# Kernel tuning notes

Hardware: AMD Instinct MI355X
Metric: run time of the kernel (lower is better)

Reference implementation:

```python
import jax, jax.numpy as jnp
import numpy as np


def setup_inputs() -> dict:
    key = jax.random.key(0)
    k1, k2 = jax.random.split(key)
    B, Te, Td, D = 8, 2048, 2048, 256
    encoder_outputs = jax.random.normal(k1, (B, Te, D), dtype=jnp.float32)
    decoder_outputs = jax.random.normal(k2, (B, Td, D), dtype=jnp.float32)
    return {"encoder_outputs": encoder_outputs, "decoder_outputs": decoder_outputs}


def reference(encoder_outputs, decoder_outputs):
    # score[b, e, t] = enc[b, e, :] . dec[b, t, :]   -> [B, Te, Td]
    score = jnp.einsum('bed,btd->bet', encoder_outputs, decoder_outputs)
    # softmax over the encoder-time axis (axis=1), matching K.softmax(..., axis=1)
    attn = jax.nn.softmax(score, axis=1)
    # context[b, t, d] = sum_e attn[b, e, t] * enc[b, e, d]
    # (original does expand_dims + broadcast-mul + sum; einsum is the same math)
    context = jnp.einsum('bet,bed->btd', attn, encoder_outputs)
    return jnp.concatenate([decoder_outputs, context], axis=-1)  # [B, Td, 2D]
```

## Files before the change

kernel.cpp:

```cpp
#include <hip/hip_runtime.h>


#define B_   8
#define TE   2048
#define TD   2048
#define D_   256
#define NIT  32

typedef _Float16 f16x8 __attribute__((ext_vector_type(8)));
typedef float f32x4 __attribute__((ext_vector_type(4)));

__device__ __forceinline__ unsigned pk2(float a, float b) {
  unsigned short ua = __builtin_bit_cast(unsigned short, (_Float16)a);
  unsigned short ub = __builtin_bit_cast(unsigned short, (_Float16)b);
  return (unsigned)ua | ((unsigned)ub << 16);
}

#define GLOAD16(gsrc, ldst)                                                  \
  __builtin_amdgcn_global_load_lds(                                          \
      (const __attribute__((address_space(1))) unsigned int*)(const void*)(gsrc), \
      (__attribute__((address_space(3))) unsigned int*)(void*)(ldst), 16, 0, 0)

__global__ __launch_bounds__(256) void prep_fused(const float* __restrict__ enc,
                                                  _Float16* __restrict__ encK,
                                                  _Float16* __restrict__ encVt) {
  __shared__ float tile[64][65];
  int bid = blockIdx.x;
  int b = bid >> 7, r = bid & 127;
  int et = r >> 2, dt = r & 3;
  int e0 = et * 64, d0 = dt * 64;
  int tx = threadIdx.x & 63, ty = threadIdx.x >> 6;
  const float* src = enc + ((size_t)b * TE + e0) * D_ + d0;
#pragma unroll
  for (int i = 0; i < 16; ++i)
    tile[i * 4 + ty][tx] = src[(size_t)(i * 4 + ty) * D_ + tx];
  __syncthreads();

  _Float16* kout = encK + ((size_t)b * TE + e0) * D_ + d0;
#pragma unroll
  for (int i = 0; i < 2; ++i) {
    int ci = i * 256 + threadIdx.x;
    int e = ci >> 3, xl = ci & 7;
    int xs = xl ^ (e & 7);
    const float* s8 = &tile[e][xs * 8];
    f16x8 h;
#pragma unroll
    for (int j = 0; j < 8; ++j) h[j] = (_Float16)s8[j];
    *(f16x8*)(kout + (size_t)e * D_ + xl * 8) = h;
  }
#pragma unroll
  for (int i = 0; i < 2; ++i) {
    int u = i * 256 + threadIdx.x;
    int y = u & 3, d_loc = (u >> 2) & 63, ctl = u >> 8;
    int s = (d_loc >> 1) & 3;
    int ebase = ctl * 32 + ((y ^ s) << 3);
    f16x8 h;
#pragma unroll
    for (int j = 0; j < 8; ++j) h[j] = (_Float16)tile[ebase + j][d_loc];
    size_t o = (((size_t)b * 64 + et * 2 + ctl) * 256 + d0 + d_loc) * 32 + y * 8;
    *(f16x8*)(encVt + o) = h;
  }
}

__global__ __launch_bounds__(512, 2) void luong_main(
    const _Float16* __restrict__ encK,
    const _Float16* __restrict__ encVt,
    const float* __restrict__ dec,
    float* __restrict__ out) {
  extern __shared__ char lds[];
  const int tid = threadIdx.x;
  const int lane = tid & 63, wave = tid >> 6;
  const int wr = wave >> 2, wc = wave & 3;
  const int g = lane >> 4, c = lane & 15;

  int bidl = (blockIdx.x & 7) * 32 + (blockIdx.x >> 3);
  const int b = bidl >> 5;
  const int q0 = (bidl & 31) * 64;
  const int t = q0 + wc * 16 + c;

  const float* decB = dec + (size_t)b * TD * D_;
  float* outB = out + (size_t)b * TD * (2 * D_);

  const _Float16* kbase = encK + ((size_t)b * TE + wr * 1024) * D_;
  const _Float16* vbase = encVt + ((size_t)b * 64 + wr * 32) * 8192;

  auto STAGE = [&](int buf, int it) {
    char* Kd = lds + (size_t)(buf * 2 + wr) * 32768;
    char* Vd = Kd + 16384;
    const _Float16* ks = kbase + (size_t)it * 8192;
    const _Float16* vs = vbase + (size_t)it * 8192;
#pragma unroll
    for (int q = 0; q < 4; ++q) {
      int chunk = wc * 256 + q * 64 + lane;
      GLOAD16(ks + (size_t)chunk * 8, Kd + wc * 4096 + q * 1024);
      GLOAD16(vs + (size_t)chunk * 8, Vd + wc * 4096 + q * 1024);
    }
  };

  STAGE(0, 0);
  STAGE(1, 1);

#pragma unroll
  for (int i = 0; i < 8; ++i) {
    int ci = tid + 512 * i;
    int rr = ci >> 6, d4 = (ci & 63) << 2;
    *(float4*)(outB + (size_t)(q0 + rr) * 512 + d4) =
        *(const float4*)(decB + (size_t)(q0 + rr) * 256 + d4);
  }

  f16x8 qh[8], ql[8];
  {
    const float* qrow = decB + (size_t)t * D_;
#pragma unroll
    for (int dc = 0; dc < 8; ++dc) {
      float4 v0 = *(const float4*)(qrow + dc * 32 + 8 * g);
      float4 v1 = *(const float4*)(qrow + dc * 32 + 8 * g + 4);
      float f[8] = {v0.x, v0.y, v0.z, v0.w, v1.x, v1.y, v1.z, v1.w};
      f16x8 H, L;
#pragma unroll
      for (int j = 0; j < 8; ++j) {
        _Float16 h = (_Float16)f[j];
        H[j] = h;
        L[j] = (_Float16)(f[j] - (float)h);
      }
      qh[dc] = H; ql[dc] = L;
    }
  }

  float m_run = -INFINITY, l_run = 0.f;
  f32x4 ctx[16];
#pragma unroll
  for (int i = 0; i < 16; ++i) ctx[i] = (f32x4){0.f, 0.f, 0.f, 0.f};

  f32x4 sA, sB;
  f16x8 bfrag;

  auto QK = [&](const char* Kb) {
    sA = (f32x4){0.f, 0.f, 0.f, 0.f};
    sB = (f32x4){0.f, 0.f, 0.f, 0.f};
    const int el0 = c, el1 = 16 + c;
#pragma unroll
    for (int dc = 0; dc < 8; ++dc) {
      int x = dc * 4 + g;
      int xsw = (x & 24) | ((x ^ el0) & 7);
      f16x8 k0 = *(const f16x8*)(Kb + el0 * 512 + (xsw << 4));
      f16x8 k1 = *(const f16x8*)(Kb + el1 * 512 + (xsw << 4));
      sA = __builtin_amdgcn_mfma_f32_16x16x32_f16(k0, qh[dc], sA, 0, 0, 0);
      sA = __builtin_amdgcn_mfma_f32_16x16x32_f16(k0, ql[dc], sA, 0, 0, 0);
      sB = __builtin_amdgcn_mfma_f32_16x16x32_f16(k1, qh[dc], sB, 0, 0, 0);
      sB = __builtin_amdgcn_mfma_f32_16x16x32_f16(k1, ql[dc], sB, 0, 0, 0);
    }
  };

  auto PV = [&](const char* Vb) {
#pragma unroll
    for (int dt = 0; dt < 16; ++dt) {
      int row = dt * 16 + c;
      f16x8 af = *(const f16x8*)(Vb + row * 64 + ((g ^ ((row >> 1) & 3)) << 4));
      ctx[dt] = __builtin_amdgcn_mfma_f32_16x16x32_f16(af, bfrag, ctx[dt], 0, 0, 0);
    }
  };

  auto SOFTMAX = [&]() {
    float vmax = fmaxf(fmaxf(fmaxf(sA[0], sA[1]), fmaxf(sA[2], sA[3])),
                       fmaxf(fmaxf(sB[0], sB[1]), fmaxf(sB[2], sB[3])));
    vmax = fmaxf(vmax, __shfl_xor(vmax, 16, 64));
    vmax = fmaxf(vmax, __shfl_xor(vmax, 32, 64));
    if (!__all(vmax <= m_run + 8.0f)) {
      float m_new = fmaxf(m_run, vmax);
      float alpha = __expf(m_run - m_new);
      l_run *= alpha;
#pragma unroll
      for (int i = 0; i < 16; ++i) ctx[i] *= alpha;
      m_run = m_new;
    }
    float p0 = __expf(sA[0] - m_run), p1 = __expf(sA[1] - m_run);
    float p2 = __expf(sA[2] - m_run), p3 = __expf(sA[3] - m_run);
    float p4 = __expf(sB[0] - m_run), p5 = __expf(sB[1] - m_run);
    float p6 = __expf(sB[2] - m_run), p7 = __expf(sB[3] - m_run);
    float ps = ((p0 + p1) + (p2 + p3)) + ((p4 + p5) + (p6 + p7));
    ps += __shfl_xor(ps, 16, 64);
    ps += __shfl_xor(ps, 32, 64);
    l_run += ps;
    unsigned w00 = pk2(p0, p1), w10 = pk2(p2, p3);
    unsigned w01 = pk2(p4, p5), w11 = pk2(p6, p7);
    int srcA = (2 * (g & 1)) * 16 + c, srcB = srcA + 16;
    int y0 = __shfl((int)w00, srcA, 64), y1 = __shfl((int)w10, srcA, 64);
    int y2 = __shfl((int)w00, srcB, 64), y3 = __shfl((int)w10, srcB, 64);
    int z0 = __shfl((int)w01, srcA, 64), z1 = __shfl((int)w11, srcA, 64);
    int z2 = __shfl((int)w01, srcB, 64), z3 = __shfl((int)w11, srcB, 64);
    int4 bi = (g >> 1) ? make_int4(z0, z1, z2, z3) : make_int4(y0, y1, y2, y3);
    bfrag = __builtin_bit_cast(f16x8, bi);
  };

  asm volatile("s_waitcnt vmcnt(8)" ::: "memory");
  __builtin_amdgcn_sched_barrier(0);
  __builtin_amdgcn_s_barrier();
  __builtin_amdgcn_sched_barrier(0);

#pragma unroll 2
  for (int it = 0; it < NIT; ++it) {
    const int cur = it & 1;
    const char* bufC = lds + (size_t)(cur * 2 + wr) * 32768;

    __builtin_amdgcn_s_setprio(1);
    QK(bufC);
    __builtin_amdgcn_s_setprio(0);
    SOFTMAX();
    __builtin_amdgcn_s_setprio(1);
    PV(bufC + 16384);
    __builtin_amdgcn_s_setprio(0);

    asm volatile("s_waitcnt lgkmcnt(0)" ::: "memory");
    __builtin_amdgcn_sched_barrier(0);
    __builtin_amdgcn_s_barrier();
    __builtin_amdgcn_sched_barrier(0);

    if (it + 2 < NIT) {
      STAGE(cur, it + 2);
      asm volatile("s_waitcnt vmcnt(8)" ::: "memory");
    } else {
      asm volatile("s_waitcnt vmcnt(0)" ::: "memory");
    }
    __builtin_amdgcn_sched_barrier(0);
    __builtin_amdgcn_s_barrier();
    __builtin_amdgcn_sched_barrier(0);
  }

  float* mlb = (float*)(lds + 130048);
  if (lane < 16) {
    mlb[((wr * 4 + wc) * 16 + c) * 2 + 0] = m_run;
    mlb[((wr * 4 + wc) * 16 + c) * 2 + 1] = l_run;
  }
  __syncthreads();
  float m_o = mlb[(((1 - wr) * 4 + wc) * 16 + c) * 2 + 0];
  float l_o = mlb[(((1 - wr) * 4 + wc) * 16 + c) * 2 + 1];
  float M = fmaxf(m_run, m_o);
  float fme = __expf(m_run - M);
  float L = l_run * fme + l_o * __expf(m_o - M);
  float invL = 1.0f / L;

  float* Xb = (float*)lds + wc * 4352;
  if (wr == 1) {
#pragma unroll
    for (int dt = 0; dt < 16; ++dt)
#pragma unroll
      for (int r = 0; r < 4; ++r) {
        int d = dt * 16 + 4 * g + r;
        Xb[d * 17 + c] = ctx[dt][r] * fme;
      }
  }
  __syncthreads();
  if (wr == 0) {
    float* orow = outB + (size_t)t * 512 + 256;
#pragma unroll
    for (int dt = 0; dt < 16; ++dt) {
      float4 v;
      float vv[4];
#pragma unroll
      for (int r = 0; r < 4; ++r) {
        int d = dt * 16 + 4 * g + r;
        vv[r] = (ctx[dt][r] * fme + Xb[d * 17 + c]) * invL;
      }
      v.x = vv[0]; v.y = vv[1]; v.z = vv[2]; v.w = vv[3];
      *(float4*)(orow + dt * 16 + 4 * g) = v;
    }
  }
}

extern "C" void kernel_launch(void* const* d_in, const int* in_sizes, int n_in,
                              void* d_out, int out_size, void* d_ws, size_t ws_size,
                              hipStream_t stream) {
  const float* enc = (const float*)d_in[0];
  const float* dec = (const float*)d_in[1];
  float* out = (float*)d_out;
  (void)in_sizes; (void)n_in; (void)out_size; (void)ws_size;

  _Float16* encK  = (_Float16*)d_ws;
  _Float16* encVt = (_Float16*)((char*)d_ws + 8388608);

  prep_fused<<<1024, 256, 0, stream>>>(enc, encK, encVt);
  luong_main<<<256, 512, 131072, stream>>>(encK, encVt, dec, out);
}
```

Measured before the change: 157.3 us.

## Restructure attention main loop: 2 query tiles per wave, K prefetch, 16x16x16 PV

Halves the block to 4 waves, each handling two 16-row query tiles so every K/V fragment read from LDS feeds twice as many MFMAs. The QK product for the next iteration is issued before the softmax and PV of the current one, with a triple-buffered K ring and a double-buffered V ring. This software-pipelines the loop and removes the shuffle-based P transpose by using 16x16x16 MFMAs with a re-laid-out V tile. Register pressure rises sharply (two ctx accumulators per wave) and LDS per block grows to 160KB, which lowers occupancy to one block per CU.

```diff
diff --git a/kernel.cpp b/kernel.cpp
--- a/kernel.cpp
+++ b/kernel.cpp
@@ -8,6 +8,7 @@
 #define NIT  32
 
 typedef _Float16 f16x8 __attribute__((ext_vector_type(8)));
+typedef _Float16 f16x4 __attribute__((ext_vector_type(4)));
 typedef float f32x4 __attribute__((ext_vector_type(4)));
 
 __device__ __forceinline__ unsigned pk2(float a, float b) {
@@ -51,18 +52,20 @@
 #pragma unroll
   for (int i = 0; i < 2; ++i) {
     int u = i * 256 + threadIdx.x;
-    int y = u & 3, d_loc = (u >> 2) & 63, ctl = u >> 8;
-    int s = (d_loc >> 1) & 3;
-    int ebase = ctl * 32 + ((y ^ s) << 3);
+    int gpos = u & 3, d_loc = (u >> 2) & 63, ctl = u >> 8;
+    int gs = gpos ^ ((d_loc >> 1) & 3);
+    int eb = ctl * 32 + 4 * gs;
     f16x8 h;
 #pragma unroll
-    for (int j = 0; j < 8; ++j) h[j] = (_Float16)tile[ebase + j][d_loc];
-    size_t o = (((size_t)b * 64 + et * 2 + ctl) * 256 + d0 + d_loc) * 32 + y * 8;
+    for (int j = 0; j < 4; ++j) h[j] = (_Float16)tile[eb + j][d_loc];
+#pragma unroll
+    for (int j = 0; j < 4; ++j) h[4 + j] = (_Float16)tile[eb + 16 + j][d_loc];
+    size_t o = (((size_t)b * 64 + et * 2 + ctl) * 256 + d0 + d_loc) * 32 + gpos * 8;
     *(f16x8*)(encVt + o) = h;
   }
 }
 
-__global__ __launch_bounds__(512, 2) void luong_main(
+__global__ __launch_bounds__(256, 1) void luong_main(
     const _Float16* __restrict__ encK,
     const _Float16* __restrict__ encVt,
     const float* __restrict__ dec,
@@ -70,13 +73,13 @@
   extern __shared__ char lds[];
   const int tid = threadIdx.x;
   const int lane = tid & 63, wave = tid >> 6;
-  const int wr = wave >> 2, wc = wave & 3;
+  const int wr = wave >> 1, tw = wave & 1;
   const int g = lane >> 4, c = lane & 15;
 
   int bidl = (blockIdx.x & 7) * 32 + (blockIdx.x >> 3);
   const int b = bidl >> 5;
   const int q0 = (bidl & 31) * 64;
-  const int t = q0 + wc * 16 + c;
+  const int tbase = q0 + tw * 32;
 
   const float* decB = dec + (size_t)b * TD * D_;
   float* outB = out + (size_t)b * TD * (2 * D_);
@@ -84,33 +87,38 @@
   const _Float16* kbase = encK + ((size_t)b * TE + wr * 1024) * D_;
   const _Float16* vbase = encVt + ((size_t)b * 64 + wr * 32) * 8192;
 
-  auto STAGE = [&](int buf, int it) {
-    char* Kd = lds + (size_t)(buf * 2 + wr) * 32768;
-    char* Vd = Kd + 16384;
-    const _Float16* ks = kbase + (size_t)it * 8192;
-    const _Float16* vs = vbase + (size_t)it * 8192;
-#pragma unroll
-    for (int q = 0; q < 4; ++q) {
-      int chunk = wc * 256 + q * 64 + lane;
-      GLOAD16(ks + (size_t)chunk * 8, Kd + wc * 4096 + q * 1024);
-      GLOAD16(vs + (size_t)chunk * 8, Vd + wc * 4096 + q * 1024);
-    }
+  char* grpK = lds + (size_t)wr * 81920;
+  char* grpV = grpK + 49152;
+
+  auto KSTAGE = [&](int slot, int it) {
+    char* Kd = grpK + slot * 16384 + tw * 8192;
+    const _Float16* ks = kbase + (size_t)it * 8192 + tw * 4096;
+#pragma unroll
+    for (int q = 0; q < 8; ++q)
+      GLOAD16(ks + q * 512 + lane * 8, Kd + q * 1024);
   };
-
-  STAGE(0, 0);
-  STAGE(1, 1);
-
-#pragma unroll
-  for (int i = 0; i < 8; ++i) {
-    int ci = tid + 512 * i;
+  auto VSTAGE = [&](int slot, int it) {
+    char* Vd = grpV + slot * 16384 + tw * 8192;
+    const _Float16* vs = vbase + (size_t)it * 8192 + tw * 4096;
+#pragma unroll
+    for (int q = 0; q < 8; ++q)
+      GLOAD16(vs + q * 512 + lane * 8, Vd + q * 1024);
+  };
+
+  KSTAGE(0, 0); VSTAGE(0, 0); KSTAGE(1, 1); VSTAGE(1, 1); KSTAGE(2, 2);
+
+#pragma unroll
+  for (int i = 0; i < 16; ++i) {
+    int ci = tid + 256 * i;
     int rr = ci >> 6, d4 = (ci & 63) << 2;
     *(float4*)(outB + (size_t)(q0 + rr) * 512 + d4) =
         *(const float4*)(decB + (size_t)(q0 + rr) * 256 + d4);
   }
 
-  f16x8 qh[8], ql[8];
-  {
-    const float* qrow = decB + (size_t)t * D_;
+  f16x8 qh[2][8], ql[2][8];
+#pragma unroll
+  for (int tt = 0; tt < 2; ++tt) {
+    const float* qrow = decB + (size_t)(tbase + tt * 16 + c) * D_;
 #pragma unroll
     for (int dc = 0; dc < 8; ++dc) {
       float4 v0 = *(const float4*)(qrow + dc * 32 + 8 * g);
@@ -123,147 +131,178 @@
         H[j] = h;
         L[j] = (_Float16)(f[j] - (float)h);
       }
-      qh[dc] = H; ql[dc] = L;
-    }
-  }
-
-  float m_run = -INFINITY, l_run = 0.f;
-  f32x4 ctx[16];
-#pragma unroll
-  for (int i = 0; i < 16; ++i) ctx[i] = (f32x4){0.f, 0.f, 0.f, 0.f};
-
-  f32x4 sA, sB;
-  f16x8 bfrag;
-
-  auto QK = [&](const char* Kb) {
-    sA = (f32x4){0.f, 0.f, 0.f, 0.f};
-    sB = (f32x4){0.f, 0.f, 0.f, 0.f};
-    const int el0 = c, el1 = 16 + c;
-#pragma unroll
-    for (int dc = 0; dc < 8; ++dc) {
-      int x = dc * 4 + g;
-      int xsw = (x & 24) | ((x ^ el0) & 7);
-      f16x8 k0 = *(const f16x8*)(Kb + el0 * 512 + (xsw << 4));
-      f16x8 k1 = *(const f16x8*)(Kb + el1 * 512 + (xsw << 4));
-      sA = __builtin_amdgcn_mfma_f32_16x16x32_f16(k0, qh[dc], sA, 0, 0, 0);
-      sA = __builtin_amdgcn_mfma_f32_16x16x32_f16(k0, ql[dc], sA, 0, 0, 0);
-      sB = __builtin_amdgcn_mfma_f32_16x16x32_f16(k1, qh[dc], sB, 0, 0, 0);
-      sB = __builtin_amdgcn_mfma_f32_16x16x32_f16(k1, ql[dc], sB, 0, 0, 0);
-    }
-  };
-
-  auto PV = [&](const char* Vb) {
-#pragma unroll
-    for (int dt = 0; dt < 16; ++dt) {
-      int row = dt * 16 + c;
-      f16x8 af = *(const f16x8*)(Vb + row * 64 + ((g ^ ((row >> 1) & 3)) << 4));
-      ctx[dt] = __builtin_amdgcn_mfma_f32_16x16x32_f16(af, bfrag, ctx[dt], 0, 0, 0);
-    }
-  };
-
-  auto SOFTMAX = [&]() {
-    float vmax = fmaxf(fmaxf(fmaxf(sA[0], sA[1]), fmaxf(sA[2], sA[3])),
-                       fmaxf(fmaxf(sB[0], sB[1]), fmaxf(sB[2], sB[3])));
-    vmax = fmaxf(vmax, __shfl_xor(vmax, 16, 64));
-    vmax = fmaxf(vmax, __shfl_xor(vmax, 32, 64));
-    if (!__all(vmax <= m_run + 8.0f)) {
-      float m_new = fmaxf(m_run, vmax);
-      float alpha = __expf(m_run - m_new);
-      l_run *= alpha;
-#pragma unroll
-      for (int i = 0; i < 16; ++i) ctx[i] *= alpha;
-      m_run = m_new;
-    }
-    float p0 = __expf(sA[0] - m_run), p1 = __expf(sA[1] - m_run);
-    float p2 = __expf(sA[2] - m_run), p3 = __expf(sA[3] - m_run);
-    float p4 = __expf(sB[0] - m_run), p5 = __expf(sB[1] - m_run);
-    float p6 = __expf(sB[2] - m_run), p7 = __expf(sB[3] - m_run);
-    float ps = ((p0 + p1) + (p2 + p3)) + ((p4 + p5) + (p6 + p7));
-    ps += __shfl_xor(ps, 16, 64);
-    ps += __shfl_xor(ps, 32, 64);
-    l_run += ps;
-    unsigned w00 = pk2(p0, p1), w10 = pk2(p2, p3);
-    unsigned w01 = pk2(p4, p5), w11 = pk2(p6, p7);
-    int srcA = (2 * (g & 1)) * 16 + c, srcB = srcA + 16;
-    int y0 = __shfl((int)w00, srcA, 64), y1 = __shfl((int)w10, srcA, 64);
-    int y2 = __shfl((int)w00, srcB, 64), y3 = __shfl((int)w10, srcB, 64);
-    int z0 = __shfl((int)w01, srcA, 64), z1 = __shfl((int)w11, srcA, 64);
-    int z2 = __shfl((int)w01, srcB, 64), z3 = __shfl((int)w11, srcB, 64);
-    int4 bi = (g >> 1) ? make_int4(z0, z1, z2, z3) : make_int4(y0, y1, y2, y3);
-    bfrag = __builtin_bit_cast(f16x8, bi);
-  };
-
-  asm volatile("s_waitcnt vmcnt(8)" ::: "memory");
+      qh[tt][dc] = H; ql[tt][dc] = L;
+    }
+  }
+
+  asm volatile("s_waitcnt vmcnt(0)" ::: "memory");
   __builtin_amdgcn_sched_barrier(0);
   __builtin_amdgcn_s_barrier();
   __builtin_amdgcn_sched_barrier(0);
 
-#pragma unroll 2
+  float m_run[2] = {-INFINITY, -INFINITY}, l_run[2] = {0.f, 0.f};
+  f32x4 ctx[2][16];
+#pragma unroll
+  for (int tt = 0; tt < 2; ++tt)
+#pragma unroll
+    for (int i = 0; i < 16; ++i) ctx[tt][i] = (f32x4){0.f, 0.f, 0.f, 0.f};
+
+  f32x4 sA[2], sB[2];
+
+  auto QK = [&](int slot, f32x4 oA[2], f32x4 oB[2]) {
+    const char* Kb = grpK + slot * 16384;
+#pragma unroll
+    for (int tt = 0; tt < 2; ++tt) {
+      oA[tt] = (f32x4){0.f, 0.f, 0.f, 0.f};
+      oB[tt] = (f32x4){0.f, 0.f, 0.f, 0.f};
+    }
+#pragma unroll
+    for (int dc = 0; dc < 8; ++dc) {
+      int x = dc * 4 + g;
+      int xsw = (x & 24) | ((x ^ c) & 7);
+      f16x8 k0 = *(const f16x8*)(Kb + c * 512 + (xsw << 4));
+      f16x8 k1 = *(const f16x8*)(Kb + (16 + c) * 512 + (xsw << 4));
+#pragma unroll
+      for (int tt = 0; tt < 2; ++tt) {
+        oA[tt] = __builtin_amdgcn_mfma_f32_16x16x32_f16(k0, qh[tt][dc], oA[tt], 0, 0, 0);
+        oA[tt] = __builtin_amdgcn_mfma_f32_16x16x32_f16(k0, ql[tt][dc], oA[tt], 0, 0, 0);
+        oB[tt] = __builtin_amdgcn_mfma_f32_16x16x32_f16(k1, qh[tt][dc], oB[tt], 0, 0, 0);
+        oB[tt] = __builtin_amdgcn_mfma_f32_16x16x32_f16(k1, ql[tt][dc], oB[tt], 0, 0, 0);
+      }
+    }
+  };
+
+  QK(0, sA, sB);
+
+  int kslot_rd = 1, kslot_wr = 0;
+
   for (int it = 0; it < NIT; ++it) {
-    const int cur = it & 1;
-    const char* bufC = lds + (size_t)(cur * 2 + wr) * 32768;
-
-    __builtin_amdgcn_s_setprio(1);
-    QK(bufC);
-    __builtin_amdgcn_s_setprio(0);
-    SOFTMAX();
-    __builtin_amdgcn_s_setprio(1);
-    PV(bufC + 16384);
-    __builtin_amdgcn_s_setprio(0);
-
-    asm volatile("s_waitcnt lgkmcnt(0)" ::: "memory");
+    const bool hasNext = (it + 1 < NIT);
+    f32x4 nA[2], nB[2];
+    if (hasNext) QK(kslot_rd, nA, nB);
+
+    f16x4 bfA[2], bfB[2];
+    {
+      float vx[2];
+#pragma unroll
+      for (int tt = 0; tt < 2; ++tt) {
+        float v = fmaxf(fmaxf(fmaxf(sA[tt][0], sA[tt][1]), fmaxf(sA[tt][2], sA[tt][3])),
+                        fmaxf(fmaxf(sB[tt][0], sB[tt][1]), fmaxf(sB[tt][2], sB[tt][3])));
+        v = fmaxf(v, __shfl_xor(v, 16, 64));
+        v = fmaxf(v, __shfl_xor(v, 32, 64));
+        vx[tt] = v;
+      }
+      bool need = (vx[0] > m_run[0] + 8.0f) || (vx[1] > m_run[1] + 8.0f);
+      if (__any(need)) {
+#pragma unroll
+        for (int tt = 0; tt < 2; ++tt) {
+          float mn = fmaxf(m_run[tt], vx[tt]);
+          float alpha = __expf(m_run[tt] - mn);
+          l_run[tt] *= alpha;
+#pragma unroll
+          for (int i = 0; i < 16; ++i) ctx[tt][i] *= alpha;
+          m_run[tt] = mn;
+        }
+      }
+#pragma unroll
+      for (int tt = 0; tt < 2; ++tt) {
+        float p0 = __expf(sA[tt][0] - m_run[tt]), p1 = __expf(sA[tt][1] - m_run[tt]);
+        float p2 = __expf(sA[tt][2] - m_run[tt]), p3 = __expf(sA[tt][3] - m_run[tt]);
+        float p4 = __expf(sB[tt][0] - m_run[tt]), p5 = __expf(sB[tt][1] - m_run[tt]);
+        float p6 = __expf(sB[tt][2] - m_run[tt]), p7 = __expf(sB[tt][3] - m_run[tt]);
+        float ps = ((p0 + p1) + (p2 + p3)) + ((p4 + p5) + (p6 + p7));
+        ps += __shfl_xor(ps, 16, 64);
+        ps += __shfl_xor(ps, 32, 64);
+        l_run[tt] += ps;
+        bfA[tt] = __builtin_bit_cast(f16x4, make_int2((int)pk2(p0, p1), (int)pk2(p2, p3)));
+        bfB[tt] = __builtin_bit_cast(f16x4, make_int2((int)pk2(p4, p5), (int)pk2(p6, p7)));
+      }
+    }
+
+    {
+      const char* Vb = grpV + (it & 1) * 16384;
+#pragma unroll
+      for (int dt = 0; dt < 16; ++dt) {
+        int row = dt * 16 + c;
+        f16x8 v8 = *(const f16x8*)(Vb + row * 64 + ((g ^ ((row >> 1) & 3)) << 4));
+        int4 vi = __builtin_bit_cast(int4, v8);
+        f16x4 a0 = __builtin_bit_cast(f16x4, make_int2(vi.x, vi.y));
+        f16x4 a1 = __builtin_bit_cast(f16x4, make_int2(vi.z, vi.w));
+        ctx[0][dt] = __builtin_amdgcn_mfma_f32_16x16x16f16(a0, bfA[0], ctx[0][dt], 0, 0, 0);
+        ctx[0][dt] = __builtin_amdgcn_mfma_f32_16x16x16f16(a1, bfB[0], ctx[0][dt], 0, 0, 0);
+        ctx[1][dt] = __builtin_amdgcn_mfma_f32_16x16x16f16(a0, bfA[1], ctx[1][dt], 0, 0, 0);
+        ctx[1][dt] = __builtin_amdgcn_mfma_f32_16x16x16f16(a1, bfB[1], ctx[1][dt], 0, 0, 0);
+      }
+    }
+
+    if (hasNext) {
+#pragma unroll
+      for (int tt = 0; tt < 2; ++tt) { sA[tt] = nA[tt]; sB[tt] = nB[tt]; }
+    }
+
+    asm volatile("s_waitcnt vmcnt(0) lgkmcnt(0)" ::: "memory");
     __builtin_amdgcn_sched_barrier(0);
     __builtin_amdgcn_s_barrier();
     __builtin_amdgcn_sched_barrier(0);
 
-    if (it + 2 < NIT) {
-      STAGE(cur, it + 2);
-      asm volatile("s_waitcnt vmcnt(8)" ::: "memory");
-    } else {
-      asm volatile("s_waitcnt vmcnt(0)" ::: "memory");
-    }
+    if (it + 3 < NIT) KSTAGE(kslot_wr, it + 3);
+    if (it + 2 < NIT) VSTAGE(it & 1, it + 2);
     __builtin_amdgcn_sched_barrier(0);
-    __builtin_amdgcn_s_barrier();
-    __builtin_amdgcn_sched_barrier(0);
-  }
-
-  float* mlb = (float*)(lds + 130048);
-  if (lane < 16) {
-    mlb[((wr * 4 + wc) * 16 + c) * 2 + 0] = m_run;
-    mlb[((wr * 4 + wc) * 16 + c) * 2 + 1] = l_run;
-  }
+
+    kslot_wr = kslot_rd;
+    kslot_rd = (kslot_rd >= 2) ? 0 : kslot_rd + 1;
+  }
+
   __syncthreads();
-  float m_o = mlb[(((1 - wr) * 4 + wc) * 16 + c) * 2 + 0];
-  float l_o = mlb[(((1 - wr) * 4 + wc) * 16 + c) * 2 + 1];
-  float M = fmaxf(m_run, m_o);
-  float fme = __expf(m_run - M);
-  float L = l_run * fme + l_o * __expf(m_o - M);
-  float invL = 1.0f / L;
-
-  float* Xb = (float*)lds + wc * 4352;
+  float* mlb = (float*)(lds + 65536);
+  if (g == 0) {
+#pragma unroll
+    for (int tt = 0; tt < 2; ++tt) {
+      int idx = wr * 64 + tw * 32 + tt * 16 + c;
+      mlb[idx * 2 + 0] = m_run[tt];
+      mlb[idx * 2 + 1] = l_run[tt];
+    }
+  }
+  __syncthreads();
+  float fme[2], invL[2];
+#pragma unroll
+  for (int tt = 0; tt < 2; ++tt) {
+    int idx_o = (1 - wr) * 64 + tw * 32 + tt * 16 + c;
+    float mo = mlb[idx_o * 2 + 0], lo = mlb[idx_o * 2 + 1];
+    float M = fmaxf(m_run[tt], mo);
+    fme[tt] = __expf(m_run[tt] - M);
+    float L = l_run[tt] * fme[tt] + lo * __expf(mo - M);
+    invL[tt] = 1.0f / L;
+  }
+
+  float* Xb = (float*)lds;
   if (wr == 1) {
 #pragma unroll
-    for (int dt = 0; dt < 16; ++dt)
-#pragma unroll
-      for (int r = 0; r < 4; ++r) {
-        int d = dt * 16 + 4 * g + r;
-        Xb[d * 17 + c] = ctx[dt][r] * fme;
-      }
+    for (int tt = 0; tt < 2; ++tt)
+#pragma unroll
+      for (int dt = 0; dt < 16; ++dt)
+#pragma unroll
+        for (int r = 0; r < 4; ++r) {
+          int d = dt * 16 + 4 * g + r;
+          Xb[d * 64 + tw * 32 + tt * 16 + c] = ctx[tt][dt][r] * fme[tt];
+        }
   }
   __syncthreads();
   if (wr == 0) {
-    float* orow = outB + (size_t)t * 512 + 256;
-#pragma unroll
-    for (int dt = 0; dt < 16; ++dt) {
-      float4 v;
-      float vv[4];
-#pragma unroll
-      for (int r = 0; r < 4; ++r) {
-        int d = dt * 16 + 4 * g + r;
-        vv[r] = (ctx[dt][r] * fme + Xb[d * 17 + c]) * invL;
-      }
-      v.x = vv[0]; v.y = vv[1]; v.z = vv[2]; v.w = vv[3];
-      *(float4*)(orow + dt * 16 + 4 * g) = v;
+#pragma unroll
+    for (int tt = 0; tt < 2; ++tt) {
+      float* orow = outB + (size_t)(tbase + tt * 16 + c) * 512 + 256;
+#pragma unroll
+      for (int dt = 0; dt < 16; ++dt) {
+        float vv[4];
+#pragma unroll
+        for (int r = 0; r < 4; ++r) {
+          int d = dt * 16 + 4 * g + r;
+          vv[r] = (ctx[tt][dt][r] * fme[tt] + Xb[d * 64 + tw * 32 + tt * 16 + c]) * invL[tt];
+        }
+        float4 v; v.x = vv[0]; v.y = vv[1]; v.z = vv[2]; v.w = vv[3];
+        *(float4*)(orow + dt * 16 + 4 * g) = v;
+      }
     }
   }
 }
@@ -280,5 +319,5 @@
   _Float16* encVt = (_Float16*)((char*)d_ws + 8388608);
 
   prep_fused<<<1024, 256, 0, stream>>>(enc, encK, encVt);
-  luong_main<<<256, 512, 131072, stream>>>(encK, encVt, dec, out);
+  luong_main<<<256, 256, 163840, stream>>>(encK, encVt, dec, out);
 }
```

Measured after the change: 175.7 us. 11.7% more time.
